# Optimization experiments

Measured on AMD Instinct MI355X. Metric: run time of the kernel, lower is better.

Reference implementation:

```python
import jax, jax.numpy as jnp
import numpy as np

TEMPERATURE = 0.07
BASE_TEMPERATURE = 0.07


def setup_inputs() -> dict:
    key = jax.random.key(0)
    k1, k2, k3, k4 = jax.random.split(key, 4)
    b, N, d = 1024, 32768, 128
    output_q = jax.random.normal(k1, (b, d), dtype=jnp.float32)
    output_q = output_q / jnp.linalg.norm(output_q, axis=1, keepdims=True)
    queue_all = jax.random.normal(k2, (b + N, d), dtype=jnp.float32)
    queue_all = queue_all / jnp.linalg.norm(queue_all, axis=1, keepdims=True)
    # class flags in [-1, 20); -1 means 'invalid / ignore' per the module's special-casing
    flags = jax.random.randint(k3, (b, 1), -1, 20, dtype=jnp.int32)
    queue_flags_all = jax.random.randint(k4, (b + N, 1), -1, 20, dtype=jnp.int32)
    return {
        "output_q": output_q,
        "queue_all": queue_all,
        "flags": flags,
        "queue_flags_all": queue_flags_all,
        "n_iter": 100,
    }


def reference(output_q, queue_all, flags, queue_flags_all, n_iter):
    b = output_q.shape[0]
    queue = queue_all[b:]            # [N, d]
    qflags = queue_flags_all[b:]     # [N, 1]
    # anchor-vs-queue logits, max-subtracted for stability (max is detached)
    logits = (output_q @ queue.T) / TEMPERATURE                       # [b, N]
    logits = logits - jax.lax.stop_gradient(jnp.max(logits, axis=1, keepdims=True))
    # positive mask: same flag; rows with flag == -1 are fully zeroed
    row_m1 = flags[:, 0] == -1                                        # [b]
    mask_pos = (flags == qflags.T) & (~row_m1[:, None])               # [b, N]
    logits = jnp.where(row_m1[:, None], 0.0, logits)
    lfp = logits * mask_pos                                           # logits_filtered_pos
    if n_iter >= 0:
        # per-row flag revision: if far more entries below the row mean than above,
        # the row's pseudo-label is deemed wrong -> flag := 0, positives zeroed
        mean_sim = lfp.mean(axis=1, keepdims=True)                    # [b, 1]
        pos_cnt = jnp.sum(lfp >= mean_sim, axis=1).astype(jnp.float32)
        wrong_cnt = jnp.sum(lfp < mean_sim, axis=1).astype(jnp.float32)
        revise = (wrong_cnt / (pos_cnt + 1e-6)) > 10.0                # [b]
        flags = jnp.where(revise[:, None], 0, flags)
        lfp = jnp.where(revise[:, None], 0.0, lfp)
    # zero out queue columns whose flag is -1
    col_m1 = qflags[:, 0] == -1                                       # [N]
    logits = jnp.where(col_m1[None, :], 0.0, logits)
    exp_logits = jnp.exp(logits)
    # exact-zero logits (masked entries AND the natural row max) give exp == 1 -> drop them
    exp_logits = exp_logits * (exp_logits != 1.0)
    row_sum = exp_logits.sum(axis=1, keepdims=True)                   # [b, 1]
    log_prob = lfp - jnp.log(row_sum + 1e-12)                         # [b, N]
    num_nonzero = jnp.sum(lfp != 0.0).astype(jnp.float32)             # global count (scalar)
    row_lp = log_prob.sum(axis=1)                                     # [b]
    cond = (num_nonzero > 0) & (row_sum[:, 0] > 0) & (row_lp < 0)     # per-row gate
    loss = jnp.sum(jnp.where(cond, row_lp / num_nonzero, 0.0)) / b
    loss = -(TEMPERATURE / BASE_TEMPERATURE) * loss
    return loss.reshape(1), flags
```

## Files before the change

kernel.cpp:

```cpp
#include <hip/hip_runtime.h>
#include <stdint.h>


typedef short bf16x8 __attribute__((ext_vector_type(8)));
typedef unsigned short ushort8v __attribute__((ext_vector_type(8)));
typedef float f32x4 __attribute__((ext_vector_type(4)));

#define INV_T 14.285714285714286f
#define K2E 20.609929155698604f

__device__ __forceinline__ unsigned short f2bf(float x) {
    unsigned u = __float_as_uint(x);
    return (unsigned short)((u + 0x7FFFu + ((u >> 16) & 1u)) >> 16);
}
__device__ __forceinline__ ushort8v cvt8(const float4* s4) {
    float4 a = s4[0], b = s4[1];
    ushort8v v;
    v[0] = f2bf(a.x); v[1] = f2bf(a.y); v[2] = f2bf(a.z); v[3] = f2bf(a.w);
    v[4] = f2bf(b.x); v[5] = f2bf(b.y); v[6] = f2bf(b.z); v[7] = f2bf(b.w);
    return v;
}
__device__ __forceinline__ void gload_lds16(const void* g, void* l) {
    __builtin_amdgcn_global_load_lds(
        (const __attribute__((address_space(1))) unsigned int*)g,
        (__attribute__((address_space(3))) unsigned int*)l, 16, 0, 0);
}

__global__ void convert_kernel(const float* __restrict__ Q,
                               const float* __restrict__ Kv,
                               const int* __restrict__ qf,
                               unsigned short* __restrict__ Qb,
                               char* __restrict__ KbB,
                               unsigned* __restrict__ histP,
                               unsigned* __restrict__ wrongA, int N, int b) {
    __shared__ unsigned lh[32];
    const int t = threadIdx.x;
    const int blk = blockIdx.x;
    if (blk < 64) {
        if (t < 32) lh[t] = 0u;
        __syncthreads();
        int j0 = blk * 512;
        atomicAdd(&lh[qf[j0 + t] + 1], 1u);
        atomicAdd(&lh[qf[j0 + 256 + t] + 1], 1u);
        __syncthreads();
        if (t < 32) histP[blk * 32 + t] = lh[t];
    }
    int i = blk * 256 + t;
    if (i < b) wrongA[i] = 0u;
    int nk = N * 16;
    if (i < nk) {
        int row = i >> 4, kc = i & 15;
        ushort8v v = cvt8(reinterpret_cast<const float4*>(
            Kv + (size_t)row * 128 + kc * 8));
        int tb = row >> 6, rr = row & 63;
        int off = tb * 16384 + ((rr * 256 + kc * 16) ^ ((rr & 7) << 4));
        *reinterpret_cast<ushort8v*>(KbB + off) = v;
    } else if (i < nk + b * 16) {
        int j = i - nk;
        int row = j >> 4, kc = j & 15;
        ushort8v v = cvt8(reinterpret_cast<const float4*>(
            Q + (size_t)row * 128 + kc * 8));
        *reinterpret_cast<ushort8v*>((char*)Qb + row * 256 + kc * 16) = v;
    }
}

__global__ __launch_bounds__(512, 2) void gemm_kernel(
    const unsigned short* __restrict__ Qb, const char* __restrict__ KbB,
    const int* __restrict__ flags, const int* __restrict__ qf,
    float4* __restrict__ part, int b)
{
    __shared__ __align__(16) char sB[2][16384];
    const int tid = threadIdx.x;
    const int lane = tid & 63, g = lane >> 4, q = lane & 15;
    const int wave = tid >> 6, wr = wave >> 1, wc = wave & 1;
    const int bx = blockIdx.x;
    const int r0 = blockIdx.y * 128;

    bf16x8 af[2][4];
#pragma unroll
    for (int mi = 0; mi < 2; ++mi) {
        int row = r0 + 32 * wr + 16 * mi + q;
#pragma unroll
        for (int ks = 0; ks < 4; ++ks)
            af[mi][ks] = *reinterpret_cast<const bf16x8*>(
                Qb + (size_t)row * 128 + ks * 32 + g * 8);
    }
    unsigned flpack[2];
#pragma unroll
    for (int mi = 0; mi < 2; ++mi) {
        unsigned p = 0;
#pragma unroll
        for (int reg = 0; reg < 4; ++reg) {
            int f = flags[r0 + 32 * wr + 16 * mi + 4 * g + reg];
            unsigned byte = (f < 0) ? 255u : (unsigned)(f + 1);
            p |= byte << (8 * reg);
        }
        flpack[mi] = p;
    }

    float bestp[8], se[8], sl[8];
#pragma unroll
    for (int r = 0; r < 8; ++r) { bestp[r] = -3.0e38f; se[r] = 0.f; sl[r] = 0.f; }

#define STAGE(buf, gt)                                                 \
    {                                                                  \
        const char* s_ = KbB + (size_t)(gt) * 16384 + tid * 16;        \
        char* d_ = &sB[buf][tid * 16];                                 \
        gload_lds16(s_, d_);                                           \
        gload_lds16(s_ + 8192, d_ + 8192);                             \
    }

    STAGE(0, bx * 8);

    for (int t = 0; t < 8; ++t) {
        __syncthreads();
        if (t < 7) STAGE((t + 1) & 1, bx * 8 + t + 1);
        const char* bb = sB[t & 1];

        f32x4 acc[2][2];
#pragma unroll
        for (int mi = 0; mi < 2; ++mi)
#pragma unroll
            for (int ni = 0; ni < 2; ++ni) acc[mi][ni] = (f32x4){0, 0, 0, 0};

#pragma unroll
        for (int ks = 0; ks < 4; ++ks) {
            bf16x8 bf[2];
#pragma unroll
            for (int ni = 0; ni < 2; ++ni) {
                int rr = 32 * wc + 16 * ni + q;
                bf[ni] = *reinterpret_cast<const bf16x8*>(
                    bb + ((rr * 256 + ks * 64 + g * 16) ^ ((rr & 7) << 4)));
            }
#pragma unroll
            for (int mi = 0; mi < 2; ++mi)
#pragma unroll
                for (int ni = 0; ni < 2; ++ni)
                    acc[mi][ni] = __builtin_amdgcn_mfma_f32_16x16x32_bf16(
                        af[mi][ks], bf[ni], acc[mi][ni], 0, 0, 0);
        }

        int cb = bx * 512 + t * 64 + 32 * wc + q;
        unsigned qv1[2] = {(unsigned)(qf[cb] + 1), (unsigned)(qf[cb + 16] + 1)};
        float bias[2] = {(qv1[0] == 0u) ? -1024.f : 0.f,
                         (qv1[1] == 0u) ? -1024.f : 0.f};
#pragma unroll
        for (int mi = 0; mi < 2; ++mi)
#pragma unroll
            for (int reg = 0; reg < 4; ++reg) {
                int rr8 = mi * 4 + reg;
                unsigned fc = (flpack[mi] >> (8 * reg)) & 255u;
                float bp = bestp[rr8], s = se[rr8], l = sl[rr8];
#pragma unroll
                for (int ni = 0; ni < 2; ++ni) {
                    float dot = acc[mi][ni][reg];
                    s += exp2f(__builtin_fmaf(dot, K2E, bias[ni]));
                    l += (qv1[ni] == fc) ? dot : 0.f;
                    float dp = __uint_as_float(
                        (__float_as_uint(dot) & ~31u) | qv1[ni]);
                    bp = fmaxf(bp, dp);
                }
                bestp[rr8] = bp; se[rr8] = s; sl[rr8] = l;
            }
    }

    float4* scr = (float4*)sB;
#pragma unroll
    for (int rr8 = 0; rr8 < 8; ++rr8) {
        float bp = bestp[rr8], s = se[rr8], l = sl[rr8];
#pragma unroll
        for (int off = 1; off < 16; off <<= 1) {
            float ob = __shfl_xor(bp, off);
            float os = __shfl_xor(s, off);
            float ol = __shfl_xor(l, off);
            bp = fmaxf(bp, ob);
            s += os;
            l += ol;
        }
        if (q == 0) {
            int rl = 32 * wr + 16 * (rr8 >> 2) + 4 * g + (rr8 & 3);
            scr[wc * 128 + rl] = make_float4(bp, s, l, 0.f);
        }
    }
    __syncthreads();
    if (tid < 128) {
        float4 a = scr[tid], c = scr[128 + tid];
        part[(size_t)bx * b + r0 + tid] =
            make_float4(fmaxf(a.x, c.x), a.y + c.y, a.z + c.z, 0.f);
    }
}

__global__ __launch_bounds__(256) void reduce_kernel(
    const float4* __restrict__ part, const int* __restrict__ flags,
    const unsigned* __restrict__ histP, const float* __restrict__ Q,
    const float* __restrict__ Kv, const int* __restrict__ qf,
    float* __restrict__ bestA, int* __restrict__ flagsA,
    float* __restrict__ sumlA, float* __restrict__ sumexpA,
    unsigned* __restrict__ cntA, unsigned* __restrict__ wrongA, int N, int b)
{
    __shared__ float4 red[4][64];
    __shared__ unsigned sh[32];
    __shared__ float sB64[64], sL64[64];
    __shared__ unsigned sC64[64];
    __shared__ int sList[64];
    __shared__ int sNum;
    __shared__ unsigned sWp;
    __shared__ float sQrow[128];

    const int t = threadIdx.x;
    if (t == 0) sNum = 0;
    if (t < 32) {
        unsigned s = 0;
#pragma unroll
        for (int i = 0; i < 64; ++i) s += histP[i * 32 + t];
        sh[t] = s;
    }
    const int rl = t & 63;
    const int r = blockIdx.x * 64 + rl;
    const int pg = t >> 6;
    float bp = -3.0e38f, s = 0.f, l = 0.f;
    for (int cs = pg; cs < 64; cs += 4) {
        float4 p = part[(size_t)cs * b + r];
        bp = fmaxf(bp, p.x);
        s += p.y;
        l += p.z;
    }
    red[pg][rl] = make_float4(bp, s, l, 0.f);
    __syncthreads();
    if (t < 64) {
        const int rr = blockIdx.x * 64 + t;
        bp = -3.0e38f; s = 0.f; l = 0.f;
#pragma unroll
        for (int i = 0; i < 4; ++i) {
            float4 p = red[i][t];
            bp = fmaxf(bp, p.x);
            s += p.y;
            l += p.z;
        }
        bestA[rr] = bp;
        flagsA[rr] = (int)(__float_as_uint(bp) & 31u);
        sumexpA[rr] = s;
        sumlA[rr] = l;
        int f = flags[rr];
        unsigned c = (f >= 0) ? sh[f + 1] : 0u;
        cntA[rr] = c;
        sB64[t] = bp; sL64[t] = l; sC64[t] = c;
        float ub = (float)c / ((float)(N - (int)c) + 1e-6f);
        if (ub > 10.0f) {
            int slot = atomicAdd(&sNum, 1);
            sList[slot] = t;
        }
    }
    __syncthreads();
    const int nt = sNum;
    for (int i = 0; i < nt; ++i) {
        int rloc = sList[i];
        int rr = blockIdx.x * 64 + rloc;
        if (t == 0) sWp = 0u;
        if (t < 128) sQrow[t] = Q[(size_t)rr * 128 + t];
        __syncthreads();
        float m = sB64[rloc] * INV_T;
        unsigned c = sC64[rloc];
        float mean = (INV_T * sL64[rloc] - (float)c * m) / (float)N;
        int f = flags[rr];
        int wp = 0;
        for (int j = t; j < N; j += 256) {
            float dot = 0.f;
            const float* kr = Kv + (size_t)j * 128;
            for (int k = 0; k < 128; ++k) dot += sQrow[k] * kr[k];
            bool mask = (f == qf[j]) && (f != -1);
            float lfp = mask ? (dot * INV_T - m) : 0.f;
            if (lfp < mean) wp++;
        }
        atomicAdd(&sWp, (unsigned)wp);
        __syncthreads();
        if (t == 0) wrongA[rr] = sWp;
        __syncthreads();
    }
}

__global__ __launch_bounds__(1024) void final_kernel(
    const int* __restrict__ flags, const int* __restrict__ n_iter_p,
    const float* __restrict__ bestA, const int* __restrict__ flagsA,
    const float* __restrict__ sumlA, const float* __restrict__ sumexpA,
    const unsigned* __restrict__ cntA, const unsigned* __restrict__ wrongA,
    float* __restrict__ out, int N, int b)
{
    __shared__ unsigned swU[16];
    __shared__ float swF[16];
    __shared__ unsigned sTot;
    const int r = threadIdx.x;
    const int lane = r & 63, wv = r >> 6;

    int f = flags[r];
    bool row_m1 = (f == -1);
    float mdot = bestA[r];
    float m = mdot * INV_T;
    int qmax1 = flagsA[r];
    float s = sumexpA[r];
    float l = sumlA[r];
    unsigned cnt = cntA[r];

    float rowsum;
    if (row_m1) {
        rowsum = 0.f;
    } else {
        float adj = s - ((qmax1 == 0) ? 0.f : exp2f(mdot * K2E));
        rowsum = exp2f(-mdot * K2E) * adj;
        rowsum = fmaxf(rowsum, 0.f);
    }
    float sum_lfp = INV_T * l - (float)cnt * m;
    bool ispos = (!row_m1) && (qmax1 - 1 == f);
    unsigned nnz = cnt - (ispos ? 1u : 0u);

    int nit = *n_iter_p;
    bool revise = false;
    if (nit >= 0) {
        float ub = (float)cnt / ((float)(N - (int)cnt) + 1e-6f);
        if (ub > 10.0f) {
            unsigned wr = wrongA[r];
            float wf = (float)wr;
            float pf = (float)(N - (int)wr);
            revise = (wf / (pf + 1e-6f)) > 10.0f;
        }
    }
    out[1 + r] = (float)(revise ? 0 : f);
    float eff_suml = revise ? 0.f : sum_lfp;
    unsigned eff_nnz = revise ? 0u : nnz;

    unsigned nn = eff_nnz;
#pragma unroll
    for (int off = 1; off < 64; off <<= 1) nn += __shfl_xor(nn, off);
    if (lane == 0) swU[wv] = nn;
    __syncthreads();
    if (r == 0) {
        unsigned tot = 0;
#pragma unroll
        for (int i = 0; i < 16; ++i) tot += swU[i];
        sTot = tot;
    }
    __syncthreads();
    unsigned total_nnz = sTot;

    float row_lp = eff_suml - (float)N * logf(rowsum + 1e-12f);
    float contrib = (total_nnz > 0u && rowsum > 0.f && row_lp < 0.f)
                        ? row_lp / (float)total_nnz
                        : 0.f;
#pragma unroll
    for (int off = 1; off < 64; off <<= 1) contrib += __shfl_xor(contrib, off);
    if (lane == 0) swF[wv] = contrib;
    __syncthreads();
    if (r == 0) {
        float tot = 0.f;
#pragma unroll
        for (int i = 0; i < 16; ++i) tot += swF[i];
        out[0] = -(tot / (float)b);
    }
}

extern "C" void kernel_launch(void* const* d_in, const int* in_sizes, int n_in,
                              void* d_out, int out_size, void* d_ws,
                              size_t ws_size, hipStream_t stream)
{
    const float* Q = (const float*)d_in[0];
    const float* Kall = (const float*)d_in[1];
    const int* flags = (const int*)d_in[2];
    const int* qfall = (const int*)d_in[3];
    const int* n_iter = (const int*)d_in[4];
    float* out = (float*)d_out;

    const int b = in_sizes[2];
    const int total = in_sizes[3];
    const int N = total - b;
    const float* Kv = Kall + (size_t)b * 128;
    const int* qf = qfall + b;

    char* wsb = (char*)d_ws;
    float* bestA = (float*)wsb;
    int* flagsA = (int*)(wsb + 4096);
    float* sumlA = (float*)(wsb + 8192);
    float* sumexpA = (float*)(wsb + 12288);
    unsigned* cntA = (unsigned*)(wsb + 16384);
    unsigned* wrongA = (unsigned*)(wsb + 20480);
    unsigned* histP = (unsigned*)(wsb + 24576);
    float4* part = (float4*)(wsb + 32768);
    char* KbB = wsb + 32768 + (size_t)64 * b * 16;
    unsigned short* Qb = (unsigned short*)(KbB + (size_t)N * 256);

    int nconv = (N + b) * 16;
    convert_kernel<<<(nconv + 255) / 256, 256, 0, stream>>>(
        Q, Kv, qf, Qb, KbB, histP, wrongA, N, b);

    dim3 grid(N / 512, b / 128);
    gemm_kernel<<<grid, 512, 0, stream>>>(Qb, KbB, flags, qf, part, b);
    reduce_kernel<<<b / 64, 256, 0, stream>>>(part, flags, histP, Q, Kv, qf,
                                              bestA, flagsA, sumlA, sumexpA,
                                              cntA, wrongA, N, b);
    final_kernel<<<1, b, 0, stream>>>(flags, n_iter, bestA, flagsA, sumlA,
                                      sumexpA, cntA, wrongA, out, N, b);
}
```

Before: 44.17 us.

## Fuse reduce and final kernels into GEMM tail via last-block atomic counter

Removes the separate reduce and final kernel launches. The last GEMM block to finish, detected with an atomic done counter plus thread fences, does the cross-tile reduction, the flag-revision scan and the loss. The GEMM also preloads queue flags into packed registers and fully unrolls the tile loop. The cost is that the final reduction and any revise scans run serially on a single 512-thread block instead of 16 blocks, and the extra shared memory and registers may hurt occupancy.

```diff
diff --git a/kernel.cpp b/kernel.cpp
--- a/kernel.cpp
+++ b/kernel.cpp
@@ -32,10 +32,11 @@
                                unsigned short* __restrict__ Qb,
                                char* __restrict__ KbB,
                                unsigned* __restrict__ histP,
-                               unsigned* __restrict__ wrongA, int N, int b) {
+                               unsigned* __restrict__ done, int N, int b) {
     __shared__ unsigned lh[32];
     const int t = threadIdx.x;
     const int blk = blockIdx.x;
+    if (blk == 0 && t == 0) *done = 0u;
     if (blk < 64) {
         if (t < 32) lh[t] = 0u;
         __syncthreads();
@@ -46,7 +47,6 @@
         if (t < 32) histP[blk * 32 + t] = lh[t];
     }
     int i = blk * 256 + t;
-    if (i < b) wrongA[i] = 0u;
     int nk = N * 16;
     if (i < nk) {
         int row = i >> 4, kc = i & 15;
@@ -66,10 +66,20 @@
 
 __global__ __launch_bounds__(512, 2) void gemm_kernel(
     const unsigned short* __restrict__ Qb, const char* __restrict__ KbB,
+    const float* __restrict__ Qf, const float* __restrict__ Kvf,
     const int* __restrict__ flags, const int* __restrict__ qf,
-    float4* __restrict__ part, int b)
+    const int* __restrict__ n_iter_p, float4* __restrict__ part,
+    const unsigned* __restrict__ histP, unsigned* __restrict__ done,
+    float* __restrict__ out, int N, int b)
 {
     __shared__ __align__(16) char sB[2][16384];
+    __shared__ unsigned sh[32];
+    __shared__ int sNum;
+    __shared__ unsigned sLastFlag;
+    __shared__ unsigned sU[8];
+    __shared__ float sF[8];
+    __shared__ unsigned sTotN;
+
     const int tid = threadIdx.x;
     const int lane = tid & 63, g = lane >> 4, q = lane & 15;
     const int wave = tid >> 6, wr = wave >> 1, wc = wave & 1;
@@ -96,6 +106,19 @@
             p |= byte << (8 * reg);
         }
         flpack[mi] = p;
+    }
+    unsigned qpack[4];
+#pragma unroll
+    for (int w = 0; w < 4; ++w) {
+        unsigned p = 0;
+#pragma unroll
+        for (int bvi = 0; bvi < 4; ++bvi) {
+            int v = w * 4 + bvi;
+            int tt = v >> 1, ni = v & 1;
+            int col = bx * 512 + tt * 64 + 32 * wc + 16 * ni + q;
+            p |= ((unsigned)(qf[col] + 1) & 255u) << (8 * bvi);
+        }
+        qpack[w] = p;
     }
 
     float bestp[8], se[8], sl[8];
@@ -112,6 +135,7 @@
 
     STAGE(0, bx * 8);
 
+#pragma unroll
     for (int t = 0; t < 8; ++t) {
         __syncthreads();
         if (t < 7) STAGE((t + 1) & 1, bx * 8 + t + 1);
@@ -140,8 +164,8 @@
                         af[mi][ks], bf[ni], acc[mi][ni], 0, 0, 0);
         }
 
-        int cb = bx * 512 + t * 64 + 32 * wc + q;
-        unsigned qv1[2] = {(unsigned)(qf[cb] + 1), (unsigned)(qf[cb + 16] + 1)};
+        unsigned qv1[2] = {(qpack[t >> 1] >> (((2 * t) & 3) * 8)) & 255u,
+                           (qpack[t >> 1] >> (((2 * t + 1) & 3) * 8)) & 255u};
         float bias[2] = {(qv1[0] == 0u) ? -1024.f : 0.f,
                          (qv1[1] == 0u) ? -1024.f : 0.f};
 #pragma unroll
@@ -188,172 +212,144 @@
         part[(size_t)bx * b + r0 + tid] =
             make_float4(fmaxf(a.x, c.x), a.y + c.y, a.z + c.z, 0.f);
     }
-}
-
-__global__ __launch_bounds__(256) void reduce_kernel(
-    const float4* __restrict__ part, const int* __restrict__ flags,
-    const unsigned* __restrict__ histP, const float* __restrict__ Q,
-    const float* __restrict__ Kv, const int* __restrict__ qf,
-    float* __restrict__ bestA, int* __restrict__ flagsA,
-    float* __restrict__ sumlA, float* __restrict__ sumexpA,
-    unsigned* __restrict__ cntA, unsigned* __restrict__ wrongA, int N, int b)
-{
-    __shared__ float4 red[4][64];
-    __shared__ unsigned sh[32];
-    __shared__ float sB64[64], sL64[64];
-    __shared__ unsigned sC64[64];
-    __shared__ int sList[64];
-    __shared__ int sNum;
-    __shared__ unsigned sWp;
-    __shared__ float sQrow[128];
-
-    const int t = threadIdx.x;
-    if (t == 0) sNum = 0;
-    if (t < 32) {
+
+    __threadfence();
+    if (tid == 0) {
+        unsigned old = atomicAdd(done, 1u);
+        sLastFlag = (old == gridDim.x * gridDim.y - 1) ? 1u : 0u;
+        sNum = 0;
+    }
+    __syncthreads();
+    if (!sLastFlag) return;
+    __threadfence();
+
+    char* base = &sB[0][0];
+    float* sBp = (float*)base;
+    float* sSl = (float*)(base + 4096);
+    float* sQrow = (float*)(base + 8192);
+    int* sList = (int*)(base + 8704);
+    unsigned* sWrong = (unsigned*)(base + 12800);
+
+    if (tid < 32) {
         unsigned s = 0;
 #pragma unroll
-        for (int i = 0; i < 64; ++i) s += histP[i * 32 + t];
-        sh[t] = s;
-    }
-    const int rl = t & 63;
-    const int r = blockIdx.x * 64 + rl;
-    const int pg = t >> 6;
-    float bp = -3.0e38f, s = 0.f, l = 0.f;
-    for (int cs = pg; cs < 64; cs += 4) {
-        float4 p = part[(size_t)cs * b + r];
-        bp = fmaxf(bp, p.x);
-        s += p.y;
-        l += p.z;
-    }
-    red[pg][rl] = make_float4(bp, s, l, 0.f);
-    __syncthreads();
-    if (t < 64) {
-        const int rr = blockIdx.x * 64 + t;
-        bp = -3.0e38f; s = 0.f; l = 0.f;
-#pragma unroll
-        for (int i = 0; i < 4; ++i) {
-            float4 p = red[i][t];
-            bp = fmaxf(bp, p.x);
-            s += p.y;
-            l += p.z;
-        }
-        bestA[rr] = bp;
-        flagsA[rr] = (int)(__float_as_uint(bp) & 31u);
-        sumexpA[rr] = s;
-        sumlA[rr] = l;
+        for (int i = 0; i < 64; ++i) s += histP[i * 32 + tid];
+        sh[tid] = s;
+    }
+    const int rA = tid, rB = tid + 512;
+    float bpA = -3.0e38f, seA = 0.f, slA = 0.f;
+    float bpB = -3.0e38f, seB = 0.f, slB = 0.f;
+    for (int cs = 0; cs < 64; ++cs) {
+        float4 pa = part[(size_t)cs * b + rA];
+        float4 pb = part[(size_t)cs * b + rB];
+        bpA = fmaxf(bpA, pa.x); seA += pa.y; slA += pa.z;
+        bpB = fmaxf(bpB, pb.x); seB += pb.y; slB += pb.z;
+    }
+    __syncthreads();
+    sBp[rA] = bpA; sSl[rA] = slA;
+    sBp[rB] = bpB; sSl[rB] = slB;
+
+    const int fA = flags[rA], fB = flags[rB];
+    __syncthreads();
+    unsigned cntA = (fA >= 0) ? sh[fA + 1] : 0u;
+    unsigned cntB = (fB >= 0) ? sh[fB + 1] : 0u;
+    float ubA = (float)cntA / ((float)(N - (int)cntA) + 1e-6f);
+    float ubB = (float)cntB / ((float)(N - (int)cntB) + 1e-6f);
+    const int nit = *n_iter_p;
+    if (nit >= 0 && ubA > 10.0f) sList[atomicAdd(&sNum, 1)] = rA;
+    if (nit >= 0 && ubB > 10.0f) sList[atomicAdd(&sNum, 1)] = rB;
+    __syncthreads();
+    const int nt = sNum;
+    for (int i = 0; i < nt; ++i) {
+        int rr = sList[i];
+        if (tid == 0) sWrong[i] = 0u;
+        if (tid < 128) sQrow[tid] = Qf[(size_t)rr * 128 + tid];
+        __syncthreads();
         int f = flags[rr];
         unsigned c = (f >= 0) ? sh[f + 1] : 0u;
-        cntA[rr] = c;
-        sB64[t] = bp; sL64[t] = l; sC64[t] = c;
-        float ub = (float)c / ((float)(N - (int)c) + 1e-6f);
-        if (ub > 10.0f) {
-            int slot = atomicAdd(&sNum, 1);
-            sList[slot] = t;
-        }
-    }
-    __syncthreads();
-    const int nt = sNum;
-    for (int i = 0; i < nt; ++i) {
-        int rloc = sList[i];
-        int rr = blockIdx.x * 64 + rloc;
-        if (t == 0) sWp = 0u;
-        if (t < 128) sQrow[t] = Q[(size_t)rr * 128 + t];
-        __syncthreads();
-        float m = sB64[rloc] * INV_T;
-        unsigned c = sC64[rloc];
-        float mean = (INV_T * sL64[rloc] - (float)c * m) / (float)N;
-        int f = flags[rr];
+        float m = sBp[rr] * INV_T;
+        float mean = (INV_T * sSl[rr] - (float)c * m) / (float)N;
         int wp = 0;
-        for (int j = t; j < N; j += 256) {
+        for (int j = tid; j < N; j += 512) {
             float dot = 0.f;
-            const float* kr = Kv + (size_t)j * 128;
+            const float* kr = Kvf + (size_t)j * 128;
             for (int k = 0; k < 128; ++k) dot += sQrow[k] * kr[k];
             bool mask = (f == qf[j]) && (f != -1);
             float lfp = mask ? (dot * INV_T - m) : 0.f;
             if (lfp < mean) wp++;
         }
-        atomicAdd(&sWp, (unsigned)wp);
-        __syncthreads();
-        if (t == 0) wrongA[rr] = sWp;
-        __syncthreads();
-    }
-}
-
-__global__ __launch_bounds__(1024) void final_kernel(
-    const int* __restrict__ flags, const int* __restrict__ n_iter_p,
-    const float* __restrict__ bestA, const int* __restrict__ flagsA,
-    const float* __restrict__ sumlA, const float* __restrict__ sumexpA,
-    const unsigned* __restrict__ cntA, const unsigned* __restrict__ wrongA,
-    float* __restrict__ out, int N, int b)
-{
-    __shared__ unsigned swU[16];
-    __shared__ float swF[16];
-    __shared__ unsigned sTot;
-    const int r = threadIdx.x;
-    const int lane = r & 63, wv = r >> 6;
-
-    int f = flags[r];
-    bool row_m1 = (f == -1);
-    float mdot = bestA[r];
-    float m = mdot * INV_T;
-    int qmax1 = flagsA[r];
-    float s = sumexpA[r];
-    float l = sumlA[r];
-    unsigned cnt = cntA[r];
-
-    float rowsum;
-    if (row_m1) {
-        rowsum = 0.f;
-    } else {
-        float adj = s - ((qmax1 == 0) ? 0.f : exp2f(mdot * K2E));
-        rowsum = exp2f(-mdot * K2E) * adj;
-        rowsum = fmaxf(rowsum, 0.f);
-    }
-    float sum_lfp = INV_T * l - (float)cnt * m;
-    bool ispos = (!row_m1) && (qmax1 - 1 == f);
-    unsigned nnz = cnt - (ispos ? 1u : 0u);
-
-    int nit = *n_iter_p;
-    bool revise = false;
-    if (nit >= 0) {
-        float ub = (float)cnt / ((float)(N - (int)cnt) + 1e-6f);
-        if (ub > 10.0f) {
-            unsigned wr = wrongA[r];
-            float wf = (float)wr;
-            float pf = (float)(N - (int)wr);
+        atomicAdd(&sWrong[i], (unsigned)wp);
+        __syncthreads();
+    }
+
+    float sumlfpX[2], rowsumX[2];
+    unsigned effX[2];
+    int rX[2] = {rA, rB};
+    int fX[2] = {fA, fB};
+    unsigned cX[2] = {cntA, cntB};
+    float bpX[2] = {bpA, bpB}, seX[2] = {seA, seB}, slX[2] = {slA, slB};
+    float ubX[2] = {ubA, ubB};
+#pragma unroll
+    for (int s2 = 0; s2 < 2; ++s2) {
+        int f = fX[s2];
+        bool row_m1 = (f == -1);
+        float mdot = bpX[s2];
+        float m = mdot * INV_T;
+        int qmax1 = (int)(__float_as_uint(mdot) & 31u);
+        float rowsum;
+        if (row_m1) {
+            rowsum = 0.f;
+        } else {
+            float adj = seX[s2] - ((qmax1 == 0) ? 0.f : exp2f(mdot * K2E));
+            rowsum = fmaxf(exp2f(-mdot * K2E) * adj, 0.f);
+        }
+        float sum_lfp = INV_T * slX[s2] - (float)cX[s2] * m;
+        bool ispos = (!row_m1) && (qmax1 - 1 == f);
+        unsigned nnz = cX[s2] - (ispos ? 1u : 0u);
+        bool revise = false;
+        if (nit >= 0 && ubX[s2] > 10.0f) {
+            unsigned wr2 = 0;
+            for (int i = 0; i < nt; ++i)
+                if (sList[i] == rX[s2]) wr2 = sWrong[i];
+            float wf = (float)wr2, pf = (float)(N - (int)wr2);
             revise = (wf / (pf + 1e-6f)) > 10.0f;
         }
-    }
-    out[1 + r] = (float)(revise ? 0 : f);
-    float eff_suml = revise ? 0.f : sum_lfp;
-    unsigned eff_nnz = revise ? 0u : nnz;
-
-    unsigned nn = eff_nnz;
+        out[1 + rX[s2]] = (float)(revise ? 0 : f);
+        sumlfpX[s2] = revise ? 0.f : sum_lfp;
+        effX[s2] = revise ? 0u : nnz;
+        rowsumX[s2] = rowsum;
+    }
+
+    unsigned nn = effX[0] + effX[1];
 #pragma unroll
     for (int off = 1; off < 64; off <<= 1) nn += __shfl_xor(nn, off);
-    if (lane == 0) swU[wv] = nn;
-    __syncthreads();
-    if (r == 0) {
+    if (lane == 0) sU[wave] = nn;
+    __syncthreads();
+    if (tid == 0) {
         unsigned tot = 0;
 #pragma unroll
-        for (int i = 0; i < 16; ++i) tot += swU[i];
-        sTot = tot;
-    }
-    __syncthreads();
-    unsigned total_nnz = sTot;
-
-    float row_lp = eff_suml - (float)N * logf(rowsum + 1e-12f);
-    float contrib = (total_nnz > 0u && rowsum > 0.f && row_lp < 0.f)
-                        ? row_lp / (float)total_nnz
-                        : 0.f;
+        for (int i = 0; i < 8; ++i) tot += sU[i];
+        sTotN = tot;
+    }
+    __syncthreads();
+    unsigned total_nnz = sTotN;
+
+    float contrib = 0.f;
+#pragma unroll
+    for (int s2 = 0; s2 < 2; ++s2) {
+        float row_lp = sumlfpX[s2] - (float)N * logf(rowsumX[s2] + 1e-12f);
+        contrib += (total_nnz > 0u && rowsumX[s2] > 0.f && row_lp < 0.f)
+                       ? row_lp / (float)total_nnz
+                       : 0.f;
+    }
 #pragma unroll
     for (int off = 1; off < 64; off <<= 1) contrib += __shfl_xor(contrib, off);
-    if (lane == 0) swF[wv] = contrib;
-    __syncthreads();
-    if (r == 0) {
+    if (lane == 0) sF[wave] = contrib;
+    __syncthreads();
+    if (tid == 0) {
         float tot = 0.f;
 #pragma unroll
-        for (int i = 0; i < 16; ++i) tot += swF[i];
+        for (int i = 0; i < 8; ++i) tot += sF[i];
         out[0] = -(tot / (float)b);
     }
 }
@@ -376,26 +372,17 @@
     const int* qf = qfall + b;
 
     char* wsb = (char*)d_ws;
-    float* bestA = (float*)wsb;
-    int* flagsA = (int*)(wsb + 4096);
-    float* sumlA = (float*)(wsb + 8192);
-    float* sumexpA = (float*)(wsb + 12288);
-    unsigned* cntA = (unsigned*)(wsb + 16384);
-    unsigned* wrongA = (unsigned*)(wsb + 20480);
-    unsigned* histP = (unsigned*)(wsb + 24576);
+    unsigned* done = (unsigned*)wsb;
+    unsigned* histP = (unsigned*)(wsb + 256);
     float4* part = (float4*)(wsb + 32768);
     char* KbB = wsb + 32768 + (size_t)64 * b * 16;
     unsigned short* Qb = (unsigned short*)(KbB + (size_t)N * 256);
 
     int nconv = (N + b) * 16;
     convert_kernel<<<(nconv + 255) / 256, 256, 0, stream>>>(
-        Q, Kv, qf, Qb, KbB, histP, wrongA, N, b);
+        Q, Kv, qf, Qb, KbB, histP, done, N, b);
 
     dim3 grid(N / 512, b / 128);
-    gemm_kernel<<<grid, 512, 0, stream>>>(Qb, KbB, flags, qf, part, b);
-    reduce_kernel<<<b / 64, 256, 0, stream>>>(part, flags, histP, Q, Kv, qf,
-                                              bestA, flagsA, sumlA, sumexpA,
-                                              cntA, wrongA, N, b);
-    final_kernel<<<1, b, 0, stream>>>(flags, n_iter, bestA, flagsA, sumlA,
-                                      sumexpA, cntA, wrongA, out, N, b);
-}
+    gemm_kernel<<<grid, 512, 0, stream>>>(Qb, KbB, Q, Kv, flags, qf, n_iter,
+                                          part, histP, done, out, N, b);
+}
```

Result: slower. 146.5 us (+231.7%).
